# Optimization experiments

Measured on AMD Instinct MI355X. Metric: run time of the kernel, lower is better.

Reference implementation:

```python
import jax, jax.numpy as jnp
import numpy as np

VOL_DIM = 256  # stored volume is [256,256,256,1]


def _deform(c, W1, b1, W2, b2, W3, b3, Wf, bf):
    # chain of 1x1x1 convs (== per-voxel matmuls) with cos activations, residual *5
    h = jnp.cos(jnp.einsum('...c,cd->...d', c, W1) + b1)
    h = jnp.cos(jnp.einsum('...c,cd->...d', h, W2) + b2)
    h = jnp.cos(jnp.einsum('...c,cd->...d', h, W3) + b3)
    return c + 5.0 * (jnp.einsum('...c,cd->...d', h, Wf) + bf)


def _trilinear_sample(vol, coords):
    # vol: [X,Y,Z,C]; coords: [...,3] in voxel units (identity nifti edges)
    X, Y, Z, _ = vol.shape
    hi = jnp.array([X - 1, Y - 1, Z - 1], dtype=coords.dtype)
    c = jnp.clip(coords, 0.0, hi)
    c0 = jnp.floor(c)
    f = c - c0
    i0 = c0.astype(jnp.int32)
    i1 = jnp.minimum(i0 + 1, jnp.array([X - 1, Y - 1, Z - 1], jnp.int32))
    x0, y0, z0 = i0[..., 0], i0[..., 1], i0[..., 2]
    x1, y1, z1 = i1[..., 0], i1[..., 1], i1[..., 2]
    fx, fy, fz = f[..., 0:1], f[..., 1:2], f[..., 2:3]
    gx, gy, gz = 1.0 - fx, 1.0 - fy, 1.0 - fz
    out = (vol[x0, y0, z0] * (gx * gy * gz) + vol[x1, y0, z0] * (fx * gy * gz)
         + vol[x0, y1, z0] * (gx * fy * gz) + vol[x0, y0, z1] * (gx * gy * fz)
         + vol[x1, y1, z0] * (fx * fy * gz) + vol[x1, y0, z1] * (fx * gy * fz)
         + vol[x0, y1, z1] * (gx * fy * fz) + vol[x1, y1, z1] * (fx * fy * fz))
    return out  # [...,C]


def setup_inputs() -> dict:
    key = jax.random.key(0)
    ks = jax.random.split(key, 12)
    B, P = 64, 32
    # coords in [0, 255] world==voxel units; extra intensity channel (unused by call)
    coords = jax.random.uniform(ks[0], (B, P, P, P, 3), jnp.float32) * (VOL_DIM - 1.0)
    inten = jax.random.normal(ks[1], (B, P, P, P, 1), jnp.float32)
    x = jnp.concatenate([coords, inten], axis=-1)
    s = 0.1
    return {
        'x': x,
        'W1': jax.random.normal(ks[2], (3, 32), jnp.float32) * s,
        'b1': jax.random.normal(ks[3], (32,), jnp.float32) * s,
        'W2': jax.random.normal(ks[4], (32, 32), jnp.float32) * s,
        'b2': jax.random.normal(ks[5], (32,), jnp.float32) * s,
        'W3': jax.random.normal(ks[6], (32, 32), jnp.float32) * s,
        'b3': jax.random.normal(ks[7], (32,), jnp.float32) * s,
        'Wf': jax.random.normal(ks[8], (32, 3), jnp.float32) * s,
        'bf': jax.random.normal(ks[9], (3,), jnp.float32) * s,
        'vol': jax.random.normal(ks[10], (VOL_DIM, VOL_DIM, VOL_DIM, 1), jnp.float32),
    }


def reference(x, W1, b1, W2, b2, W3, b3, Wf, bf, vol):
    c = x[..., 0:3]                                   # world coords
    c = _deform(c, W1, b1, W2, b2, W3, b3, Wf, bf)    # deformed coords
    return _trilinear_sample(vol, c)                  # [B,32,32,32,1]
```

## Files before the change

### kernel.cpp

```cpp
#include <hip/hip_runtime.h>


#define NPTS (64 * 32 * 32 * 32)
#define NBLK (NPTS / 256)
#define SSTR 40

#define BXN 86
#define BYN 128
#define BZN 86
#define NBRICK (BXN * BYN * BZN)
#define RETILE_T (NBRICK * 8)
#define RETILE_BLK (RETILE_T / 256)
#define HALO_BYTES ((size_t)NBRICK * 64)

#define NBRICK_F (86 * 256 * 86)
#define RETILE2_T (NBRICK_F * 4)
#define RETILE2_BLK (RETILE2_T / 256)
#define FULL_BYTES ((size_t)NBRICK_F * 64)
#define WPREP_BYTES 4096

typedef __attribute__((ext_vector_type(8))) short bf16x8;
typedef __attribute__((ext_vector_type(4))) short s16x4;
typedef __attribute__((ext_vector_type(4))) float f32x4;
typedef __attribute__((ext_vector_type(2))) unsigned long long u64x2;
typedef __attribute__((ext_vector_type(2))) unsigned uint2v;
typedef __attribute__((ext_vector_type(4))) unsigned uint4v;
typedef unsigned long long u64;
typedef unsigned short u16;

__device__ __forceinline__ short bf16rne(float f) {
    unsigned u = __builtin_bit_cast(unsigned, f);
    return (short)((u + 0x7fffu + ((u >> 16) & 1u)) >> 16);
}
__device__ __forceinline__ float bf16tof(short s) {
    return __builtin_bit_cast(float, ((unsigned)(unsigned short)s) << 16);
}
__device__ __forceinline__ float h2f(u16 h) {
    return (float)__builtin_bit_cast(_Float16, h);
}
__device__ __forceinline__ u16 f2h(float f) {
    return __builtin_bit_cast(u16, (_Float16)f);
}
__device__ __forceinline__ unsigned cvt_pk_bf16(float a, float b) {
    return (unsigned)(u16)bf16rne(a) | ((unsigned)(u16)bf16rne(b) << 16);
}

__global__ __launch_bounds__(256)
void retile_k(const float4* __restrict__ vol, u64* __restrict__ dst) {
    int t   = blockIdx.x * 256 + threadIdx.x;
    int q   = t & 7;
    int gz  = (t >> 3) & 63;
    int gyx = t >> 9;
    int x = ((gyx >> 7) << 2) + (q >> 1);
    int y = ((gyx & 127) << 1) + (q & 1);
    float4 v = vol[(((x << 8) + y) << 6) + gz];
    u64 r =  (u64)f2h(v.x)
          | ((u64)f2h(v.y) << 16)
          | ((u64)f2h(v.z) << 32)
          | ((u64)f2h(v.w) << 48);
    dst[t] = r;
}

__global__ __launch_bounds__(256)
void retile_halo_k(const float* __restrict__ vol, u64* __restrict__ dst) {
    int t  = blockIdx.x * 256 + threadIdx.x;
    int q  = t & 7;
    int b  = t >> 3;
    int bz = (int)((unsigned)b % 86u);
    int r  = (int)((unsigned)b / 86u);
    int by = r & 127;
    int bx = r >> 7;
    int x  = min(bx * 3 + (q >> 1), 255);
    int y  = (by << 1) + (q & 1);
    int z0 = bz * 3;
    const float* row = vol + (((x << 8) + y) << 8);
    float v0 = row[z0];
    float v1 = row[min(z0 + 1, 255)];
    float v2 = row[min(z0 + 2, 255)];
    float v3 = row[min(z0 + 3, 255)];
    u64 rr = (u64)f2h(v0)
          | ((u64)f2h(v1) << 16)
          | ((u64)f2h(v2) << 32)
          | ((u64)f2h(v3) << 48);
    dst[t] = rr;
}

__global__ __launch_bounds__(256)
void retile_full2_k(const float* __restrict__ vol, u64* __restrict__ dst,
                    const float* __restrict__ W2, const float* __restrict__ W3,
                    short* __restrict__ wsW) {
    int t  = blockIdx.x * 256 + threadIdx.x;
    int dx = t & 3;
    int b  = t >> 2;
    int bz = (int)((unsigned)b % 86u);
    int r  = (int)((unsigned)b / 86u);
    int by = r & 255;
    int bx = r >> 8;
    int x  = min(bx * 3 + dx, 255);
    int y1 = min(by + 1, 255);
    int z0 = bz * 3;
    int zl = (z0 > 252) ? 252 : z0;
    const float* row0 = vol + (((x << 8) + by) << 8) + zl;
    const float* row1 = vol + (((x << 8) + y1) << 8) + zl;
    float va[4], vb[4];
    __builtin_memcpy(va, row0, 16);
    __builtin_memcpy(vb, row1, 16);
    if (z0 == 255) {
        va[0] = va[1] = va[2] = va[3];
        vb[0] = vb[1] = vb[2] = vb[3];
    }
    u64 lo = (u64)f2h(va[0]) | ((u64)f2h(va[1]) << 16)
           | ((u64)f2h(va[2]) << 32) | ((u64)f2h(va[3]) << 48);
    u64 hi = (u64)f2h(vb[0]) | ((u64)f2h(vb[1]) << 16)
           | ((u64)f2h(vb[2]) << 32) | ((u64)f2h(vb[3]) << 48);
    u64x2 st; st.x = lo; st.y = hi;
    *(u64x2*)(dst + (b << 3) + (dx << 1)) = st;

    if (blockIdx.x == 0) {
        int tt = threadIdx.x;
        #pragma unroll
        for (int e0 = 0; e0 < 2048; e0 += 256) {
            int e = e0 + tt;
            int ly  = e >> 10, half = (e >> 9) & 1, ln = (e >> 3) & 63, j = e & 7;
            int qq  = ln >> 4, mm = ln & 15;
            const float* W = ly ? W3 : W2;
            wsW[e] = bf16rne(W[(qq * 8 + j) * 32 + half * 16 + mm]);
        }
    }
}

__global__ __launch_bounds__(256, 8)
void deform3b_k(const float4* __restrict__ x,
                const float4* __restrict__ W1,
                const float4* __restrict__ b1,
                const float*  __restrict__ b2,
                const float*  __restrict__ b3,
                const float*  __restrict__ Wf,
                const float*  __restrict__ bf_,
                const u64*    __restrict__ volh,
                const short*  __restrict__ wsW,
                float* __restrict__ out)
{
    __shared__ short lds[4 * 64 * SSTR];
    const int tid  = threadIdx.x;
    const int lane = tid & 63;
    const int wv   = tid >> 6;
    const int m16  = lane & 15;
    const int q    = lane >> 4;
    short* __restrict__ L = &lds[wv * 64 * SSTR];

    const int p = blockIdx.x * 256 + tid;

    const float4 xv = x[p];
    const float c0 = xv.x, c1 = xv.y, c2 = xv.z;

    {
        unsigned hw[4];
        #pragma unroll
        for (int j4 = 0; j4 < 8; ++j4) {
            float4 wa = W1[j4], wb = W1[8 + j4], wc = W1[16 + j4], bb = b1[j4];
            float v0 = __cosf(fmaf(c0, wa.x, fmaf(c1, wb.x, fmaf(c2, wc.x, bb.x))));
            float v1 = __cosf(fmaf(c0, wa.y, fmaf(c1, wb.y, fmaf(c2, wc.y, bb.y))));
            float v2 = __cosf(fmaf(c0, wa.z, fmaf(c1, wb.z, fmaf(c2, wc.z, bb.z))));
            float v3 = __cosf(fmaf(c0, wa.w, fmaf(c1, wb.w, fmaf(c2, wc.w, bb.w))));
            int o = (j4 & 1) * 2;
            hw[o + 0] = cvt_pk_bf16(v0, v1);
            hw[o + 1] = cvt_pk_bf16(v2, v3);
            if (j4 & 1) {
                uint4v st; st.x = hw[0]; st.y = hw[1]; st.z = hw[2]; st.w = hw[3];
                *(uint4v*)&L[lane * SSTR + (j4 - 1) * 4] = st;
            }
        }
    }
    __syncthreads();

    const bf16x8* __restrict__ wA = (const bf16x8*)wsW;

    const float* const bly[2] = { b2, b3 };
    #pragma unroll
    for (int ly = 0; ly < 2; ++ly) {
        bf16x8 A0 = wA[ly * 128 + lane];
        bf16x8 A1 = wA[ly * 128 + 64 + lane];
        const float* __restrict__ bb = bly[ly];
        const float4 blo = *(const float4*)&bb[q * 4];
        const float4 bhi = *(const float4*)&bb[16 + q * 4];

        #pragma unroll
        for (int t = 0; t < 4; ++t) {
            bf16x8 bfrag = *(const bf16x8*)&L[(t * 16 + m16) * SSTR + q * 8];
            f32x4 z = { 0.f, 0.f, 0.f, 0.f };
            f32x4 d0 = __builtin_amdgcn_mfma_f32_16x16x32_bf16(A0, bfrag, z, 0, 0, 0);
            f32x4 d1 = __builtin_amdgcn_mfma_f32_16x16x32_bf16(A1, bfrag, z, 0, 0, 0);
            unsigned a0 = cvt_pk_bf16(__cosf(d0[0] + blo.x), __cosf(d0[1] + blo.y));
            unsigned a1 = cvt_pk_bf16(__cosf(d0[2] + blo.z), __cosf(d0[3] + blo.w));
            unsigned a2 = cvt_pk_bf16(__cosf(d1[0] + bhi.x), __cosf(d1[1] + bhi.y));
            unsigned a3 = cvt_pk_bf16(__cosf(d1[2] + bhi.z), __cosf(d1[3] + bhi.w));
            uint2v s0; s0.x = a0; s0.y = a1;
            uint2v s1; s1.x = a2; s1.y = a3;
            *(uint2v*)&L[(t * 16 + m16) * SSTR + q * 4]      = s0;
            *(uint2v*)&L[(t * 16 + m16) * SSTR + 16 + q * 4] = s1;
        }
        __syncthreads();
    }

    float d0 = bf_[0], d1 = bf_[1], d2 = bf_[2];
    #pragma unroll
    for (int j4 = 0; j4 < 8; ++j4) {
        s16x4 v = *(const s16x4*)&L[lane * SSTR + j4 * 4];
        #pragma unroll
        for (int r = 0; r < 4; ++r) {
            float hv = bf16tof(v[r]);
            int ii = j4 * 4 + r;
            d0 = fmaf(hv, Wf[3*ii+0], d0);
            d1 = fmaf(hv, Wf[3*ii+1], d1);
            d2 = fmaf(hv, Wf[3*ii+2], d2);
        }
    }
    float e0 = fmaf(5.f, d0, c0);
    float e1 = fmaf(5.f, d1, c1);
    float e2 = fmaf(5.f, d2, c2);

    e0 = fminf(fmaxf(e0, 0.f), 255.f);
    e1 = fminf(fmaxf(e1, 0.f), 255.f);
    e2 = fminf(fmaxf(e2, 0.f), 255.f);
    float fl0 = floorf(e0), fl1 = floorf(e1), fl2 = floorf(e2);
    float fx = e0 - fl0, fy = e1 - fl1, fz = e2 - fl2;
    float gx = 1.f - fx, gy = 1.f - fy, gz = 1.f - fz;
    int x0 = (int)fl0, y0 = (int)fl1, z0 = (int)fl2;

    int bx = (int)((unsigned)x0 / 3u);  int lx = x0 - bx * 3;
    int bz = (int)((unsigned)z0 / 3u);  int lz = z0 - bz * 3;
    const u64* g = volh + ((((bx << 8) + y0) * 86 + bz) << 3) + (lx << 1);
    u64 g0 = g[0];
    u64 g1 = g[1];
    u64 g2 = g[2];
    u64 g3 = g[3];
    const int sh = lz * 16;
    u64 s0 = g0 >> sh, s1 = g1 >> sh, s2 = g2 >> sh, s3 = g3 >> sh;
    float v000 = h2f((u16)s0), v001 = h2f((u16)(s0 >> 16));
    float v010 = h2f((u16)s1), v011 = h2f((u16)(s1 >> 16));
    float v100 = h2f((u16)s2), v101 = h2f((u16)(s2 >> 16));
    float v110 = h2f((u16)s3), v111 = h2f((u16)(s3 >> 16));

    float r = gz * (gy * (gx*v000 + fx*v100) + fy * (gx*v010 + fx*v110))
            + fz * (gy * (gx*v001 + fx*v101) + fy * (gx*v011 + fx*v111));

    out[p] = r;
}

template <int MODE>
__global__ __launch_bounds__(256, 8)
void deform_sample_k(const float4* __restrict__ x,
                     const float4* __restrict__ W1,
                     const float4* __restrict__ b1,
                     const float*  __restrict__ W2,
                     const float*  __restrict__ b2,
                     const float*  __restrict__ W3,
                     const float*  __restrict__ b3,
                     const float*  __restrict__ Wf,
                     const float*  __restrict__ bf_,
                     const float*  __restrict__ volf,
                     const u64*    __restrict__ volh,
                     float* __restrict__ out)
{
    __shared__ short lds[4 * 64 * SSTR];
    const int tid  = threadIdx.x;
    const int lane = tid & 63;
    const int wv   = tid >> 6;
    const int m16  = lane & 15;
    const int q    = lane >> 4;
    short* __restrict__ L = &lds[wv * 64 * SSTR];

    const int p = blockIdx.x * 256 + tid;

    const float4 xv = x[p];
    const float c0 = xv.x, c1 = xv.y, c2 = xv.z;

    {
        bf16x8 hw;
        #pragma unroll
        for (int j4 = 0; j4 < 8; ++j4) {
            float4 wa = W1[j4], wb = W1[8 + j4], wc = W1[16 + j4], bb = b1[j4];
            float v0 = __cosf(fmaf(c0, wa.x, fmaf(c1, wb.x, fmaf(c2, wc.x, bb.x))));
            float v1 = __cosf(fmaf(c0, wa.y, fmaf(c1, wb.y, fmaf(c2, wc.y, bb.y))));
            float v2 = __cosf(fmaf(c0, wa.z, fmaf(c1, wb.z, fmaf(c2, wc.z, bb.z))));
            float v3 = __cosf(fmaf(c0, wa.w, fmaf(c1, wb.w, fmaf(c2, wc.w, bb.w))));
            int o = (j4 & 1) * 4;
            hw[o+0] = bf16rne(v0); hw[o+1] = bf16rne(v1);
            hw[o+2] = bf16rne(v2); hw[o+3] = bf16rne(v3);
            if (j4 & 1)
                *(bf16x8*)&L[lane * SSTR + (j4 - 1) * 4] = hw;
        }
    }
    __syncthreads();

    const float* const Wly[2] = { W2, W3 };
    const float* const bly[2] = { b2, b3 };
    #pragma unroll
    for (int ly = 0; ly < 2; ++ly) {
        const float* __restrict__ W  = Wly[ly];
        const float* __restrict__ bb = bly[ly];
        bf16x8 A0, A1;
        #pragma unroll
        for (int j = 0; j < 8; ++j) {
            A0[j] = bf16rne(W[(q * 8 + j) * 32 + m16]);
            A1[j] = bf16rne(W[(q * 8 + j) * 32 + 16 + m16]);
        }
        const float4 blo = *(const float4*)&bb[q * 4];
        const float4 bhi = *(const float4*)&bb[16 + q * 4];

        #pragma unroll
        for (int t = 0; t < 4; ++t) {
            bf16x8 bfrag = *(const bf16x8*)&L[(t * 16 + m16) * SSTR + q * 8];
            f32x4 z = { 0.f, 0.f, 0.f, 0.f };
            f32x4 d0 = __builtin_amdgcn_mfma_f32_16x16x32_bf16(A0, bfrag, z, 0, 0, 0);
            f32x4 d1 = __builtin_amdgcn_mfma_f32_16x16x32_bf16(A1, bfrag, z, 0, 0, 0);

            s16x4 w0, w1;
            w0[0] = bf16rne(__cosf(d0[0] + blo.x));
            w0[1] = bf16rne(__cosf(d0[1] + blo.y));
            w0[2] = bf16rne(__cosf(d0[2] + blo.z));
            w0[3] = bf16rne(__cosf(d0[3] + blo.w));
            w1[0] = bf16rne(__cosf(d1[0] + bhi.x));
            w1[1] = bf16rne(__cosf(d1[1] + bhi.y));
            w1[2] = bf16rne(__cosf(d1[2] + bhi.z));
            w1[3] = bf16rne(__cosf(d1[3] + bhi.w));
            *(s16x4*)&L[(t * 16 + m16) * SSTR + q * 4]      = w0;
            *(s16x4*)&L[(t * 16 + m16) * SSTR + 16 + q * 4] = w1;
        }
        __syncthreads();
    }

    float d0 = bf_[0], d1 = bf_[1], d2 = bf_[2];
    #pragma unroll
    for (int j4 = 0; j4 < 8; ++j4) {
        s16x4 v = *(const s16x4*)&L[lane * SSTR + j4 * 4];
        #pragma unroll
        for (int r = 0; r < 4; ++r) {
            float hv = bf16tof(v[r]);
            int ii = j4 * 4 + r;
            d0 = fmaf(hv, Wf[3*ii+0], d0);
            d1 = fmaf(hv, Wf[3*ii+1], d1);
            d2 = fmaf(hv, Wf[3*ii+2], d2);
        }
    }
    float e0 = fmaf(5.f, d0, c0);
    float e1 = fmaf(5.f, d1, c1);
    float e2 = fmaf(5.f, d2, c2);

    e0 = fminf(fmaxf(e0, 0.f), 255.f);
    e1 = fminf(fmaxf(e1, 0.f), 255.f);
    e2 = fminf(fmaxf(e2, 0.f), 255.f);
    float fl0 = floorf(e0), fl1 = floorf(e1), fl2 = floorf(e2);
    float fx = e0 - fl0, fy = e1 - fl1, fz = e2 - fl2;
    float gx = 1.f - fx, gy = 1.f - fy, gz = 1.f - fz;
    int x0 = (int)fl0, y0 = (int)fl1, z0 = (int)fl2;
    int x1 = min(x0 + 1, 255), y1 = min(y0 + 1, 255), z1 = min(z0 + 1, 255);

    float v000, v001, v010, v011, v100, v101, v110, v111;

    if constexpr (MODE == 3) {
        int bx = (int)((unsigned)x0 / 3u);  int lx = x0 - bx * 3;
        int bz = (int)((unsigned)z0 / 3u);  int lz = z0 - bz * 3;
        const u64* g = volh + ((((bx << 8) + y0) * 86 + bz) << 3) + (lx << 1);
        u64 g0 = g[0];
        u64 g1 = g[1];
        u64 g2 = g[2];
        u64 g3 = g[3];
        const int sh = lz * 16;
        u64 s0 = g0 >> sh, s1 = g1 >> sh, s2 = g2 >> sh, s3 = g3 >> sh;
        v000 = h2f((u16)s0);  v001 = h2f((u16)(s0 >> 16));
        v010 = h2f((u16)s1);  v011 = h2f((u16)(s1 >> 16));
        v100 = h2f((u16)s2);  v101 = h2f((u16)(s2 >> 16));
        v110 = h2f((u16)s3);  v111 = h2f((u16)(s3 >> 16));
    } else if constexpr (MODE == 2) {
        int bx = (int)((unsigned)x0 / 3u);  int lx = x0 - bx * 3;
        int by = y0 >> 1;                   int ly = y0 & 1;
        int bz = (int)((unsigned)z0 / 3u);  int lz = z0 - bz * 3;
        const char* vb = (const char*)volh;
        const int lineA = ((((bx << 7) + by) * 86) + bz) << 6;
        const int byB   = min(by + 1, 127);
        const int lineB = (ly == 0) ? lineA
                                    : (((((bx << 7) + byB) * 86) + bz) << 6);
        const int yrowB = (ly == 0) ? 1 : ((y0 == 255) ? 1 : 0);
        const int offA  = lx * 16 + ly * 8;
        const int offB  = lx * 16 + yrowB * 8;
        u64 LA0 = *(const u64*)(vb + lineA + offA);
        u64 LA1 = *(const u64*)(vb + lineA + offA + 16);
        u64 LB0 = *(const u64*)(vb + lineB + offB);
        u64 LB1 = *(const u64*)(vb + lineB + offB + 16);
        const int sh = lz * 16;
        u64 sA0 = LA0 >> sh, sA1 = LA1 >> sh, sB0 = LB0 >> sh, sB1 = LB1 >> sh;
        v000 = h2f((u16)sA0);  v001 = h2f((u16)(sA0 >> 16));
        v100 = h2f((u16)sA1);  v101 = h2f((u16)(sA1 >> 16));
        v010 = h2f((u16)sB0);  v011 = h2f((u16)(sB0 >> 16));
        v110 = h2f((u16)sB1);  v111 = h2f((u16)(sB1 >> 16));
    } else if constexpr (MODE == 1) {
        const int lz  = z0 & 3;
        const int zp  = (z0 >> 2) << 6;
        const int xp0 = ((x0 >> 2) << 19) | ((x0 & 3) << 4);
        const int xp1 = ((x1 >> 2) << 19) | ((x1 & 3) << 4);
        const int yp0 = ((y0 >> 1) << 12) | ((y0 & 1) << 3);
        const int yp1 = ((y1 >> 1) << 12) | ((y1 & 1) << 3);
        const char* vb = (const char*)volh;
        const int a00 = xp0 | yp0 | zp, a10 = xp1 | yp0 | zp;
        const int a01 = xp0 | yp1 | zp, a11 = xp1 | yp1 | zp;
        u64 L00 = *(const u64*)(vb + a00);
        u64 L10 = *(const u64*)(vb + a10);
        u64 L01 = *(const u64*)(vb + a01);
        u64 L11 = *(const u64*)(vb + a11);
        u64 H00 = 0, H10 = 0, H01 = 0, H11 = 0;
        const bool crossz = (lz == 3) && (z0 < 255);
        if (crossz) {
            H00 = *(const u64*)(vb + a00 + 64);
            H10 = *(const u64*)(vb + a10 + 64);
            H01 = *(const u64*)(vb + a01 + 64);
            H11 = *(const u64*)(vb + a11 + 64);
        }
        const int sh = lz * 16;
        const bool in_line = (lz < 3);
        auto ext = [&](u64 lo, u64 hi, float& a, float& b) {
            u64 s = lo >> sh;
            a = h2f((u16)s);
            float b_in = h2f((u16)(s >> 16));
            float b_nx = h2f((u16)hi);
            b = in_line ? b_in : (crossz ? b_nx : a);
        };
        ext(L00, H00, v000, v001);
        ext(L10, H10, v100, v101);
        ext(L01, H01, v010, v011);
        ext(L11, H11, v110, v111);
    } else {
        int b00 = (x0 << 16) | (y0 << 8);
        int b01 = (x0 << 16) | (y1 << 8);
        int b10 = (x1 << 16) | (y0 << 8);
        int b11 = (x1 << 16) | (y1 << 8);
        v000 = volf[b00 + z0]; v001 = volf[b00 + z1];
        v010 = volf[b01 + z0]; v011 = volf[b01 + z1];
        v100 = volf[b10 + z0]; v101 = volf[b10 + z1];
        v110 = volf[b11 + z0]; v111 = volf[b11 + z1];
    }

    float r = gz * (gy * (gx*v000 + fx*v100) + fy * (gx*v010 + fx*v110))
            + fz * (gy * (gx*v001 + fx*v101) + fy * (gx*v011 + fx*v111));

    out[p] = r;
}

extern "C" void kernel_launch(void* const* d_in, const int* in_sizes, int n_in,
                              void* d_out, int out_size, void* d_ws, size_t ws_size,
                              hipStream_t stream) {
    const float4* x   = (const float4*)d_in[0];
    const float4* W1  = (const float4*)d_in[1];
    const float4* b1  = (const float4*)d_in[2];
    const float*  W2  = (const float*)d_in[3];
    const float*  b2  = (const float*)d_in[4];
    const float*  W3  = (const float*)d_in[5];
    const float*  b3  = (const float*)d_in[6];
    const float*  Wf  = (const float*)d_in[7];
    const float*  bf_ = (const float*)d_in[8];
    const float*  vol = (const float*)d_in[9];
    float* out = (float*)d_out;

    const size_t needF = FULL_BYTES + WPREP_BYTES;
    const size_t needH = HALO_BYTES;
    const size_t need1 = (size_t)4194304 * 8;

    if (ws_size >= needF) {
        u64*   volh = (u64*)d_ws;
        short* wsW  = (short*)((char*)d_ws + FULL_BYTES);
        retile_full2_k<<<RETILE2_BLK, 256, 0, stream>>>(vol, volh, W2, W3, wsW);
        deform3b_k<<<NBLK, 256, 0, stream>>>(x, W1, b1, b2, b3, Wf, bf_,
                                             volh, wsW, out);
    } else if (ws_size >= needH) {
        u64* volh = (u64*)d_ws;
        retile_halo_k<<<RETILE_BLK, 256, 0, stream>>>(vol, volh);
        deform_sample_k<2><<<NBLK, 256, 0, stream>>>(x, W1, b1, W2, b2, W3, b3,
                                                     Wf, bf_, nullptr, volh, out);
    } else if (ws_size >= need1) {
        u64* volh = (u64*)d_ws;
        retile_k<<<16384, 256, 0, stream>>>((const float4*)vol, volh);
        deform_sample_k<1><<<NBLK, 256, 0, stream>>>(x, W1, b1, W2, b2, W3, b3,
                                                     Wf, bf_, nullptr, volh, out);
    } else {
        deform_sample_k<0><<<NBLK, 256, 0, stream>>>(x, W1, b1, W2, b2, W3, b3,
                                                     Wf, bf_, vol, nullptr, out);
    }
}
```

Measured before the change: 208.9 us.

## Fuse final projection into layer-3 MFMA epilogue and switch to fp16 MFMA

Layer 3 no longer writes activations back to LDS. Its cos outputs are multiplied by Wf in registers and reduced across lane groups with xor shuffles, which removes a barrier, the LDS round trip and the serial 32x3 per-thread dot product. Activations and weights also move from bf16 to fp16 MFMA for more mantissa precision at similar cost. The shuffles and redundant per-t reductions add some ALU work.

```diff
diff --git a/kernel.cpp b/kernel.cpp
--- a/kernel.cpp
+++ b/kernel.cpp
@@ -20,6 +20,7 @@
 #define WPREP_BYTES 4096
 
 typedef __attribute__((ext_vector_type(8))) short bf16x8;
+typedef __attribute__((ext_vector_type(8))) _Float16 h16x8;
 typedef __attribute__((ext_vector_type(4))) short s16x4;
 typedef __attribute__((ext_vector_type(4))) float f32x4;
 typedef __attribute__((ext_vector_type(2))) unsigned long long u64x2;
@@ -41,8 +42,8 @@
 __device__ __forceinline__ u16 f2h(float f) {
     return __builtin_bit_cast(u16, (_Float16)f);
 }
-__device__ __forceinline__ unsigned cvt_pk_bf16(float a, float b) {
-    return (unsigned)(u16)bf16rne(a) | ((unsigned)(u16)bf16rne(b) << 16);
+__device__ __forceinline__ unsigned pk_h16(float a, float b) {
+    return (unsigned)f2h(a) | ((unsigned)f2h(b) << 16);
 }
 
 __global__ __launch_bounds__(256)
@@ -124,13 +125,13 @@
             int ly  = e >> 10, half = (e >> 9) & 1, ln = (e >> 3) & 63, j = e & 7;
             int qq  = ln >> 4, mm = ln & 15;
             const float* W = ly ? W3 : W2;
-            wsW[e] = bf16rne(W[(qq * 8 + j) * 32 + half * 16 + mm]);
+            wsW[e] = (short)f2h(W[(qq * 8 + j) * 32 + half * 16 + mm]);
         }
     }
 }
 
 __global__ __launch_bounds__(256, 8)
-void deform3b_k(const float4* __restrict__ x,
+void deform3c_k(const float4* __restrict__ x,
                 const float4* __restrict__ W1,
                 const float4* __restrict__ b1,
                 const float*  __restrict__ b2,
@@ -164,8 +165,8 @@
             float v2 = __cosf(fmaf(c0, wa.z, fmaf(c1, wb.z, fmaf(c2, wc.z, bb.z))));
             float v3 = __cosf(fmaf(c0, wa.w, fmaf(c1, wb.w, fmaf(c2, wc.w, bb.w))));
             int o = (j4 & 1) * 2;
-            hw[o + 0] = cvt_pk_bf16(v0, v1);
-            hw[o + 1] = cvt_pk_bf16(v2, v3);
+            hw[o + 0] = pk_h16(v0, v1);
+            hw[o + 1] = pk_h16(v2, v3);
             if (j4 & 1) {
                 uint4v st; st.x = hw[0]; st.y = hw[1]; st.z = hw[2]; st.w = hw[3];
                 *(uint4v*)&L[lane * SSTR + (j4 - 1) * 4] = st;
@@ -176,25 +177,22 @@
 
     const bf16x8* __restrict__ wA = (const bf16x8*)wsW;
 
-    const float* const bly[2] = { b2, b3 };
-    #pragma unroll
-    for (int ly = 0; ly < 2; ++ly) {
-        bf16x8 A0 = wA[ly * 128 + lane];
-        bf16x8 A1 = wA[ly * 128 + 64 + lane];
-        const float* __restrict__ bb = bly[ly];
-        const float4 blo = *(const float4*)&bb[q * 4];
-        const float4 bhi = *(const float4*)&bb[16 + q * 4];
-
+    {
+        h16x8 A0 = __builtin_bit_cast(h16x8, wA[lane]);
+        h16x8 A1 = __builtin_bit_cast(h16x8, wA[64 + lane]);
+        const float4 blo = *(const float4*)&b2[q * 4];
+        const float4 bhi = *(const float4*)&b2[16 + q * 4];
         #pragma unroll
         for (int t = 0; t < 4; ++t) {
-            bf16x8 bfrag = *(const bf16x8*)&L[(t * 16 + m16) * SSTR + q * 8];
+            h16x8 bfrag = __builtin_bit_cast(h16x8,
+                *(const bf16x8*)&L[(t * 16 + m16) * SSTR + q * 8]);
             f32x4 z = { 0.f, 0.f, 0.f, 0.f };
-            f32x4 d0 = __builtin_amdgcn_mfma_f32_16x16x32_bf16(A0, bfrag, z, 0, 0, 0);
-            f32x4 d1 = __builtin_amdgcn_mfma_f32_16x16x32_bf16(A1, bfrag, z, 0, 0, 0);
-            unsigned a0 = cvt_pk_bf16(__cosf(d0[0] + blo.x), __cosf(d0[1] + blo.y));
-            unsigned a1 = cvt_pk_bf16(__cosf(d0[2] + blo.z), __cosf(d0[3] + blo.w));
-            unsigned a2 = cvt_pk_bf16(__cosf(d1[0] + bhi.x), __cosf(d1[1] + bhi.y));
-            unsigned a3 = cvt_pk_bf16(__cosf(d1[2] + bhi.z), __cosf(d1[3] + bhi.w));
+            f32x4 d0 = __builtin_amdgcn_mfma_f32_16x16x32_f16(A0, bfrag, z, 0, 0, 0);
+            f32x4 d1 = __builtin_amdgcn_mfma_f32_16x16x32_f16(A1, bfrag, z, 0, 0, 0);
+            unsigned a0 = pk_h16(__cosf(d0[0] + blo.x), __cosf(d0[1] + blo.y));
+            unsigned a1 = pk_h16(__cosf(d0[2] + blo.z), __cosf(d0[3] + blo.w));
+            unsigned a2 = pk_h16(__cosf(d1[0] + bhi.x), __cosf(d1[1] + bhi.y));
+            unsigned a3 = pk_h16(__cosf(d1[2] + bhi.z), __cosf(d1[3] + bhi.w));
             uint2v s0; s0.x = a0; s0.y = a1;
             uint2v s1; s1.x = a2; s1.y = a3;
             *(uint2v*)&L[(t * 16 + m16) * SSTR + q * 4]      = s0;
@@ -203,22 +201,51 @@
         __syncthreads();
     }
 
-    float d0 = bf_[0], d1 = bf_[1], d2 = bf_[2];
-    #pragma unroll
-    for (int j4 = 0; j4 < 8; ++j4) {
-        s16x4 v = *(const s16x4*)&L[lane * SSTR + j4 * 4];
+    float acc0 = 0.f, acc1 = 0.f, acc2 = 0.f;
+    {
+        h16x8 A0 = __builtin_bit_cast(h16x8, wA[128 + lane]);
+        h16x8 A1 = __builtin_bit_cast(h16x8, wA[192 + lane]);
+        const float4 blo = *(const float4*)&b3[q * 4];
+        const float4 bhi = *(const float4*)&b3[16 + q * 4];
+        const float bl[4] = { blo.x, blo.y, blo.z, blo.w };
+        const float bh[4] = { bhi.x, bhi.y, bhi.z, bhi.w };
+        float wf[8][3];
         #pragma unroll
         for (int r = 0; r < 4; ++r) {
-            float hv = bf16tof(v[r]);
-            int ii = j4 * 4 + r;
-            d0 = fmaf(hv, Wf[3*ii+0], d0);
-            d1 = fmaf(hv, Wf[3*ii+1], d1);
-            d2 = fmaf(hv, Wf[3*ii+2], d2);
-        }
-    }
-    float e0 = fmaf(5.f, d0, c0);
-    float e1 = fmaf(5.f, d1, c1);
-    float e2 = fmaf(5.f, d2, c2);
+            #pragma unroll
+            for (int c = 0; c < 3; ++c) {
+                wf[r][c]     = Wf[(q * 4 + r) * 3 + c];
+                wf[4 + r][c] = Wf[(16 + q * 4 + r) * 3 + c];
+            }
+        }
+        #pragma unroll
+        for (int t = 0; t < 4; ++t) {
+            h16x8 bfrag = __builtin_bit_cast(h16x8,
+                *(const bf16x8*)&L[(t * 16 + m16) * SSTR + q * 8]);
+            f32x4 z = { 0.f, 0.f, 0.f, 0.f };
+            f32x4 d0 = __builtin_amdgcn_mfma_f32_16x16x32_f16(A0, bfrag, z, 0, 0, 0);
+            f32x4 d1 = __builtin_amdgcn_mfma_f32_16x16x32_f16(A1, bfrag, z, 0, 0, 0);
+            float s0 = 0.f, s1 = 0.f, s2 = 0.f;
+            #pragma unroll
+            for (int r = 0; r < 4; ++r) {
+                float h = __cosf(d0[r] + bl[r]);
+                s0 = fmaf(h, wf[r][0], s0);
+                s1 = fmaf(h, wf[r][1], s1);
+                s2 = fmaf(h, wf[r][2], s2);
+                float h2 = __cosf(d1[r] + bh[r]);
+                s0 = fmaf(h2, wf[4 + r][0], s0);
+                s1 = fmaf(h2, wf[4 + r][1], s1);
+                s2 = fmaf(h2, wf[4 + r][2], s2);
+            }
+            s0 += __shfl_xor(s0, 16); s0 += __shfl_xor(s0, 32);
+            s1 += __shfl_xor(s1, 16); s1 += __shfl_xor(s1, 32);
+            s2 += __shfl_xor(s2, 16); s2 += __shfl_xor(s2, 32);
+            if (q == t) { acc0 = s0; acc1 = s1; acc2 = s2; }
+        }
+    }
+    float e0 = fmaf(5.f, acc0 + bf_[0], c0);
+    float e1 = fmaf(5.f, acc1 + bf_[1], c1);
+    float e2 = fmaf(5.f, acc2 + bf_[2], c2);
 
     e0 = fminf(fmaxf(e0, 0.f), 255.f);
     e1 = fminf(fmaxf(e1, 0.f), 255.f);
@@ -470,7 +497,7 @@
         u64*   volh = (u64*)d_ws;
         short* wsW  = (short*)((char*)d_ws + FULL_BYTES);
         retile_full2_k<<<RETILE2_BLK, 256, 0, stream>>>(vol, volh, W2, W3, wsW);
-        deform3b_k<<<NBLK, 256, 0, stream>>>(x, W1, b1, b2, b3, Wf, bf_,
+        deform3c_k<<<NBLK, 256, 0, stream>>>(x, W1, b1, b2, b3, Wf, bf_,
                                              volh, wsW, out);
     } else if (ws_size >= needH) {
         u64* volh = (u64*)d_ws;
```

Measured after the change: 206.6 us. No clear change (-1.1%).
